# Kernel optimization log

Measured on AMD Instinct MI355X. Metric: run time of the kernel, lower is better.

Reference implementation:

```python
import jax, jax.numpy as jnp
import numpy as np
from math import factorial

DEGREES = 6
REP = 10
PROJ = 64
R = 0.8
B = DEGREES + 1          # bandwidth; spherical signal grid is (2B, 2B)
M = (DEGREES + 1) ** 2   # 49 spherical-harmonic coefficients

# ---------- Wigner small-d coefficient tables (numpy, per degree) ----------

def _wigner_terms(l):
    idx_mp, idx_m, coef, pc, ps = [], [], [], [], []
    for mp in range(-l, l + 1):
        for m in range(-l, l + 1):
            pref = np.sqrt(float(factorial(l + mp) * factorial(l - mp) * factorial(l + m) * factorial(l - m)))
            for k in range(max(0, m - mp), min(l + m, l - mp) + 1):
                c = ((-1.0) ** (mp - m + k)) * pref / (
                    factorial(l + m - k) * factorial(k) * factorial(l - mp - k) * factorial(mp - m + k))
                idx_mp.append(mp + l); idx_m.append(m + l); coef.append(c)
                pc.append(2 * l + m - mp - 2 * k); ps.append(mp - m + 2 * k)
    return (np.asarray(idx_mp), np.asarray(idx_m), np.asarray(coef, np.float32),
            np.asarray(pc, np.float32), np.asarray(ps, np.float32))

_TERMS = [_wigner_terms(l) for l in range(DEGREES + 1)]


def _wigner_d(l, beta):
    """Real Wigner small-d matrix d^l_{m',m}(beta): (n, 2l+1, 2l+1)."""
    imp, im, coef, pc, ps = _TERMS[l]
    c = jnp.cos(beta / 2)[:, None]
    s = jnp.sin(beta / 2)[:, None]
    t = coef[None] * (c ** pc[None]) * (s ** ps[None])   # (n, T)
    d = jnp.zeros((beta.shape[0], 2 * l + 1, 2 * l + 1), beta.dtype)
    return d.at[:, imp, im].add(t)


def rotate_spectrum(angles, spectrum):
    """Block-diagonal complex Wigner-D multiply.
    angles: (n,3) ZYZ Euler; spectrum: (M, rep, 2) -> (Sre, Sim) each (n, M, rep)."""
    alpha, beta, gamma = angles[:, 0], angles[:, 1], angles[:, 2]
    out_re, out_im = [], []
    for l in range(DEGREES + 1):
        d = _wigner_d(l, beta)                                    # (n, 2l+1, 2l+1)
        ms = jnp.arange(-l, l + 1, dtype=angles.dtype)
        ang = ms[None, :, None] * alpha[:, None, None] + ms[None, None, :] * gamma[:, None, None]
        Dre = d * jnp.cos(ang)
        Dim = -d * jnp.sin(ang)                                   # D = e^{-i m' a} d e^{-i m g}
        blk = spectrum[l * l:(l + 1) * (l + 1)]                   # (2l+1, rep, 2)
        Sre, Sim = blk[..., 0], blk[..., 1]
        out_re.append(jnp.einsum('nij,jr->nir', Dre, Sre) - jnp.einsum('nij,jr->nir', Dim, Sim))
        out_im.append(jnp.einsum('nij,jr->nir', Dre, Sim) + jnp.einsum('nij,jr->nir', Dim, Sre))
    return jnp.concatenate(out_re, 1), jnp.concatenate(out_im, 1)


# ---------- Spherical harmonic synthesis table (numpy constant) ----------

def _sph_harm_table():
    J = 2 * B
    betas = np.pi * (2 * np.arange(J) + 1) / (4 * B)
    alphas = 2 * np.pi * np.arange(J) / J
    x, sx = np.cos(betas), np.sin(betas)
    L = DEGREES
    P = np.zeros((L + 1, L + 1, J))   # associated Legendre P[l, m] (Condon-Shortley)
    P[0, 0] = 1.0
    for m in range(1, L + 1):
        P[m, m] = -(2 * m - 1) * sx * P[m - 1, m - 1]
    for m in range(L + 1):
        if m + 1 <= L:
            P[m + 1, m] = (2 * m + 1) * x * P[m, m]
        for l in range(m + 2, L + 1):
            P[l, m] = ((2 * l - 1) * x * P[l - 1, m] - (l + m - 1) * P[l - 2, m]) / (l - m)
    Yre = np.zeros((M, J, J)); Yim = np.zeros((M, J, J))
    for l in range(L + 1):
        for m in range(0, l + 1):
            N = np.sqrt((2 * l + 1) / (4 * np.pi) * factorial(l - m) / factorial(l + m))
            pr = N * P[l, m]
            yre = pr[:, None] * np.cos(m * alphas)[None, :]
            yim = pr[:, None] * np.sin(m * alphas)[None, :]
            Yre[l * l + l + m], Yim[l * l + l + m] = yre, yim
            if m > 0:
                sgn = (-1.0) ** m
                Yre[l * l + l - m], Yim[l * l + l - m] = sgn * yre, -sgn * yim
    return jnp.asarray(Yre, jnp.float32), jnp.asarray(Yim, jnp.float32)

_YRE, _YIM = _sph_harm_table()


def s2_ifft_real(Sre, Sim):
    """f(beta,alpha) = Re[sum_lm c_lm Y_lm]: (n, rep, 2B, 2B)."""
    return jnp.einsum('nmr,mjk->nrjk', Sre, _YRE) - jnp.einsum('nmr,mjk->nrjk', Sim, _YIM)


# ---------- Orthographic sampling grid (numpy constant) ----------

def _ortho_grid(h, w, r):
    ys, xs = np.meshgrid(np.linspace(-r, r, h), np.linspace(-r, r, w), indexing='ij')
    rho = np.sqrt(xs ** 2 + ys ** 2)
    theta = np.arcsin(np.clip(rho, 0.0, 1.0))     # colatitude of front hemisphere
    phi = np.arctan2(ys, xs)                      # longitude in [-pi, pi)
    gx = phi / np.pi                              # alpha axis  -> grid x
    gy = 2 * theta / np.pi - 1                    # beta axis   -> grid y
    return jnp.asarray(np.stack([gx, gy], -1), jnp.float32)

_GRID = _ortho_grid(PROJ, PROJ, R)


def grid_sample_bilinear(img, grid):
    """F.grid_sample(mode=bilinear, padding=zeros, align_corners=False).
    img: (n,C,H,W); grid: (Ho,Wo,2) shared across batch."""
    n, C, H, W = img.shape
    gx = (grid[..., 0] + 1) * W / 2 - 0.5
    gy = (grid[..., 1] + 1) * H / 2 - 0.5
    x0 = jnp.floor(gx); y0 = jnp.floor(gy)
    wx1 = gx - x0; wx0 = 1 - wx1
    wy1 = gy - y0; wy0 = 1 - wy1

    def gather(xi, yi, w):
        valid = (xi >= 0) & (xi < W) & (yi >= 0) & (yi < H)
        xc = jnp.clip(xi, 0, W - 1).astype(jnp.int32)
        yc = jnp.clip(yi, 0, H - 1).astype(jnp.int32)
        vals = img[:, :, yc, xc]                 # (n, C, Ho, Wo)
        return vals * (w * valid)[None, None]
    return (gather(x0, y0, wx0 * wy0) + gather(x0 + 1, y0, wx1 * wy0)
            + gather(x0, y0 + 1, wx0 * wy1) + gather(x0 + 1, y0 + 1, wx1 * wy1))


def deconv_apply(x, wt, bt):
    """ConvTranspose2d(REP,1,kernel=4,stride=2,padding=1); wt torch layout (Cin,Cout,4,4)."""
    k = jnp.transpose(wt[:, :, ::-1, ::-1], (1, 0, 2, 3))   # (Cout,Cin,kh,kw), flipped
    y = jax.lax.conv_general_dilated(x, k, window_strides=(1, 1),
                                     padding=((2, 2), (2, 2)), lhs_dilation=(2, 2),
                                     dimension_numbers=('NCHW', 'OIHW', 'NCHW'))
    return y + bt[None, :, None, None]


def setup_inputs() -> dict:
    key = jax.random.key(0)
    k1, k2, k3 = jax.random.split(key, 3)
    return {
        'angles': jax.random.uniform(k1, (2048, 3), dtype=jnp.float32),
        'spectrum': jax.random.normal(k2, (M, REP, 2), dtype=jnp.float32),
        'wt': jax.random.normal(k3, (REP, 1, 4, 4), dtype=jnp.float32) * 0.1,
        'bt': jnp.zeros((1,), jnp.float32),
    }


def reference(angles, spectrum, wt, bt):
    Sre, Sim = rotate_spectrum(angles, spectrum)        # (n, M, rep) complex parts
    signal = s2_ifft_real(Sre, Sim)                     # (n, rep, 14, 14)
    projection = grid_sample_bilinear(signal, _GRID)    # (n, rep, 64, 64)
    return deconv_apply(projection, wt, bt)             # (n, 1, 128, 128)
```

## Files before the change

kernel.cpp:

```cpp
#include <hip/hip_runtime.h>
#include <math.h>

#define DEG   6
#define MM    49
#define REPC  10
#define JD    14
#define JROWS 8
#define PROJD 64

#define PI_F 3.14159265358979323846f
#define PI_D 3.14159265358979323846

#define WS_GW    0
#define WS_GIDX  17688
#define WS_PT    22112
#define WS_CS    22504
#define WS_FLAG  22700
#define INIT_MAGIC 0x5F3A9C74u

__device__ __constant__ int DOFF[8] = {0,1,10,35,84,165,286,455};
__device__ __constant__ float FACTF[13] = {
    1.f,1.f,2.f,6.f,24.f,120.f,720.f,5040.f,40320.f,362880.f,
    3628800.f,39916800.f,479001600.f};
__device__ __constant__ double FACTD[13] = {
    1.,1.,2.,6.,24.,120.,720.,5040.,40320.,362880.,3628800.,39916800.,479001600.};

__device__ inline float ipowf(float b, int e) {
    float r = 1.f, p = b;
    while (e) { if (e & 1) r *= p; p *= p; e >>= 1; }
    return r;
}

__global__ void init_tables(float* __restrict__ ws) {
    if (*(const volatile unsigned int*)(ws + WS_FLAG) == INIT_MAGIC) return;
    const int tid = blockIdx.x * 256 + threadIdx.x;

    if (tid < 4422) {
        const int ty = tid / 66, tx = tid - ty * 66;
        const int iy = ty - 1, ix = tx - 1;
        float4 wv = make_float4(0.f, 0.f, 0.f, 0.f);
        unsigned int bidx = 0u;
        if ((unsigned)iy < 64u && (unsigned)ix < 64u) {
            float ys = -0.8f + 1.6f * (float)iy / 63.f;
            float xs = -0.8f + 1.6f * (float)ix / 63.f;
            float rho = sqrtf(xs * xs + ys * ys);
            float theta = asinf(fminf(rho, 1.0f));
            float phi = atan2f(ys, xs);
            float gxp = (phi / PI_F + 1.f) * 7.f - 0.5f;
            float gyp = (2.f * theta / PI_F) * 7.f - 0.5f;
            float x0f = floorf(gxp), y0f = floorf(gyp);
            int x0 = (int)x0f, y0 = (int)y0f;
            float fx = gxp - x0f, fy = gyp - y0f;
            float wx0 = 1.f - fx, wx1 = fx, wy0 = 1.f - fy, wy1 = fy;
            int xb = x0, yb = y0;
            if (x0 < 0)            { xb = 0; wx0 = wx1; wx1 = 0.f; }
            else if (x0 >= JD - 1) { wx1 = 0.f; }
            if (y0 < 0)            { yb = 0; wy0 = wy1; wy1 = 0.f; }
            wv = make_float4(wy0*wx0, wy0*wx1, wy1*wx0, wy1*wx1);
            bidx = (unsigned int)((xb * 8 + yb) * 17);
        }
        ((float4*)(ws + WS_GW))[tid] = wv;
        ((unsigned int*)(ws + WS_GIDX))[tid] = bidx;
    }

    const int t2 = tid - 4422;
    if (t2 >= 0 && t2 < JROWS) {
        const int j = t2;
        double bj = PI_D * (2.0 * j + 1.0) / 28.0;
        double x = cos(bj), sx = sin(bj);
        double P[7][7];
        P[0][0] = 1.0;
        for (int m = 1; m <= 6; ++m) P[m][m] = -(2.0*m - 1.0) * sx * P[m-1][m-1];
        for (int m = 0; m <= 6; ++m) {
            if (m + 1 <= 6) P[m+1][m] = (2.0*m + 1.0) * x * P[m][m];
            for (int l = m + 2; l <= 6; ++l)
                P[l][m] = ((2.0*l - 1.0)*x*P[l-1][m] - (double)(l+m-1)*P[l-2][m])
                          / (double)(l - m);
        }
        for (int l = 0; l <= 6; ++l)
            for (int m = 0; m <= 6; ++m) {
                float v = 0.f;
                if (m <= l) {
                    double N = sqrt((2.0*l + 1.0)/(4.0*PI_D) * FACTD[l-m]/FACTD[l+m]);
                    v = (float)(N * P[l][m]);
                }
                ws[WS_PT + j*49 + l*7 + m] = v;
            }
    } else if (t2 >= JROWS && t2 < JROWS + JD) {
        const int k = t2 - JROWS;
        for (int mu = 0; mu <= 6; ++mu) {
            double ang = 2.0 * PI_D * (double)k * (double)mu / 14.0;
            ws[WS_CS + (k*7 + mu)*2 + 0] = (float)cos(ang);
            ws[WS_CS + (k*7 + mu)*2 + 1] = (float)sin(ang);
        }
    }
}

__device__ __forceinline__ float tap4(const float* __restrict__ T, int b, int c,
                                      float4 w) {
    int a = b + c;
    return fmaf(w.x, T[a],
           fmaf(w.y, T[a + 136],
           fmaf(w.z, T[a + 17],
                w.w * T[a + 153])));
}

__global__ __launch_bounds__(256, 8) void fused_decode(
    const float* __restrict__ angles,
    const float* __restrict__ spectrum,
    const float* __restrict__ wt,
    const float* __restrict__ bt,
    float* __restrict__ out,
    const float* __restrict__ ws) {
    const int n = blockIdx.x;
    const int tid = threadIdx.x;

    __shared__ __align__(16) float2 Ss[490];
    __shared__ __align__(16) float  T16p[2040];
    __shared__ __align__(16) float  bufU[1772];

    float*  sigL  = bufU;
    float*  dmatL = bufU + 1120;
    float2* CsL   = (float2*)(bufU + 1576);
    float*  specL = T16p;
    float2* ABL   = (float2*)T16p;
    float*  wLcS  = (float*)Ss;

    const float alpha = angles[n*3 + 0];
    const float beta  = angles[n*3 + 1];
    const float gamma = angles[n*3 + 2];

    if (tid < 245) ((float4*)specL)[tid] = ((const float4*)spectrum)[tid];
    if (tid < 49)  ((float4*)CsL)[tid]   = ((const float4*)(ws + WS_CS))[tid];

    {
        float cb = cosf(beta * 0.5f), sb = sinf(beta * 0.5f);
        float ratio = (sb * sb) / (cb * cb);
        for (int idx = tid; idx < 455; idx += 256) {
            int l = 0;
            while (idx >= DOFF[l+1]) ++l;
            int tl = 2*l + 1;
            int loc = idx - DOFF[l];
            int mp = loc / tl - l;
            int m  = loc % tl - l;
            float pref = sqrtf(FACTF[l+mp]*FACTF[l-mp]*FACTF[l+m]*FACTF[l-m]);
            int k0 = max(0, m - mp), k1 = min(l + m, l - mp);
            float p = ipowf(cb, 2*l + m - mp - 2*k0) * ipowf(sb, mp - m + 2*k0);
            float dsum = 0.f;
            for (int k = k0; k <= k1; ++k) {
                float c = pref / (FACTF[l+m-k]*FACTF[k]*FACTF[l-mp-k]*FACTF[mp-m+k]);
                if ((mp - m + k) & 1) c = -c;
                dsum += c * p;
                p *= ratio;
            }
            dmatL[idx] = dsum;
        }
    }
    __syncthreads();

    {
        float cg, sg; sincosf(gamma, &sg, &cg);
        for (int idx = tid; idx < 490; idx += 256) {
            int lm = idx / 10, r = idx - lm*10;
            int l = 0; { while ((l+1)*(l+1) <= lm) ++l; }
            int mp = lm - l*l - l;
            int tl = 2*l + 1;
            const float* drow = dmatL + DOFF[l] + (mp + l)*tl;
            float ca, sa; sincosf((float)mp*alpha - (float)l*gamma, &sa, &ca);
            float sre = 0.f, sim = 0.f;
            const float* sp = specL + (l*l)*20 + r*2;
            for (int mi = 0; mi < tl; ++mi) {
                float d = drow[mi];
                float Dre = d * ca, Dim = -d * sa;
                float vr = sp[mi*20], vi = sp[mi*20 + 1];
                sre += Dre*vr - Dim*vi;
                sim += Dre*vi + Dim*vr;
                float ca2 = ca*cg - sa*sg;
                float sa2 = sa*cg + ca*sg;
                ca = ca2; sa = sa2;
            }
            Ss[lm*10 + r] = make_float2(sre, sim);
        }
    }
    __syncthreads();

    for (int idx = tid; idx < 560; idx += 256) {
        int r = idx % 10;
        int jm = idx / 10;
        int j = jm / 7, mu = jm - j*7;
        float sgn = (mu & 1) ? -1.f : 1.f;
        const float* pt = ws + WS_PT + j*49 + mu;
        float A = 0.f, B = 0.f;
        #pragma unroll
        for (int l = 0; l <= 6; ++l) {
            float P = pt[l*7];
            int base = l*l + l;
            int im = base - mu; im = im < 0 ? 0 : im;
            float2 spv = Ss[(base + mu)*10 + r];
            float2 snv = Ss[im*10 + r];
            A += P * (spv.x + sgn*snv.x);
            B += P * (sgn*snv.y - spv.y);
        }
        float sc = (mu == 0) ? 0.5f : 1.f;
        ABL[idx] = make_float2(A*sc, B*sc);
    }
    __syncthreads();

    if (tid < 40) ((float4*)wLcS)[tid] = ((const float4*)wt)[tid];
    for (int idx = tid; idx < 1120; idx += 256) {
        int k = idx % 14;
        int t = idx / 14;
        int j = t & 7, r = t >> 3;
        const float2* ab = ABL + j*70 + r;
        const float2* cs = CsL + k*7;
        float acc = 0.f;
        #pragma unroll
        for (int mu = 0; mu <= 6; ++mu) {
            float2 a = ab[mu*10];
            float2 c = cs[mu];
            acc += a.x*c.x + a.y*c.y;
        }
        sigL[idx] = acc;
    }
    __syncthreads();

    for (int idx = tid; idx < 1920; idx += 256) {
        int c = idx & 15, p = idx >> 4;
        int j = p / 15, k = p - j*15;
        float acc = 0.f;
        if (k < 14) {
            const float* sl = sigL + j*14 + k;
            const float* wc = wLcS + c;
            #pragma unroll
            for (int r = 0; r < REPC; ++r)
                acc += wc[r*16] * sl[r*112];
        }
        T16p[(k*8 + j)*17 + c] = acc;
    }
    __syncthreads();

    const float btv = bt[0];
    const int wv   = tid >> 6;
    const int lane = tid & 63;
    const int pxp  = wv & 1;
    const int qy0  = wv >> 1;
    const int qx   = 2*lane + pxp;
    const int ixh  = lane + pxp;
    const int kxh  = 1 - pxp;
    const int kyh  = 1 - qy0;
    const int iyh0 = qy0;
    const int cN0 = kyh*4 + kxh, cN1 = cN0 + 2;
    const int cO0 = cN0 + 8,     cO1 = cN0 + 10;

    const unsigned int* gI = (const unsigned int*)(ws + WS_GIDX);
    const float4* gWt = (const float4*)(ws + WS_GW);

    int ridx = iyh0 * 66 + (ixh + 1);
    float4 wA0 = gWt[ridx];   unsigned int bA0 = gI[ridx];
    float4 wB0 = gWt[ridx-1]; unsigned int bB0 = gI[ridx-1];
    ridx += 66;
    float4 wA1 = gWt[ridx];   unsigned int bA1 = gI[ridx];
    float4 wB1 = gWt[ridx-1]; unsigned int bB1 = gI[ridx-1];
    ridx += 66;
    float4 wA2 = gWt[ridx];   unsigned int bA2 = gI[ridx];
    float4 wB2 = gWt[ridx-1]; unsigned int bB2 = gI[ridx-1];

    float* op = out + (size_t)n * 16384 + qy0 * 128 + qx;

    for (int t = 0; t < 63; t += 3) {
        {
            float o = btv + tap4(T16p, bA1, cN0, wA1) + tap4(T16p, bB1, cN1, wB1)
                          + tap4(T16p, bA0, cO0, wA0) + tap4(T16p, bB0, cO1, wB0);
            __builtin_nontemporal_store(o, op); op += 256;
            ridx += 66;
            wA0 = gWt[ridx]; bA0 = gI[ridx]; wB0 = gWt[ridx-1]; bB0 = gI[ridx-1];
        }
        {
            float o = btv + tap4(T16p, bA2, cN0, wA2) + tap4(T16p, bB2, cN1, wB2)
                          + tap4(T16p, bA1, cO0, wA1) + tap4(T16p, bB1, cO1, wB1);
            __builtin_nontemporal_store(o, op); op += 256;
            ridx += 66;
            wA1 = gWt[ridx]; bA1 = gI[ridx]; wB1 = gWt[ridx-1]; bB1 = gI[ridx-1];
        }
        {
            float o = btv + tap4(T16p, bA0, cN0, wA0) + tap4(T16p, bB0, cN1, wB0)
                          + tap4(T16p, bA2, cO0, wA2) + tap4(T16p, bB2, cO1, wB2);
            __builtin_nontemporal_store(o, op); op += 256;
            ridx += 66;
            wA2 = gWt[ridx]; bA2 = gI[ridx]; wB2 = gWt[ridx-1]; bB2 = gI[ridx-1];
        }
    }
    {
        float o = btv + tap4(T16p, bA1, cN0, wA1) + tap4(T16p, bB1, cN1, wB1)
                      + tap4(T16p, bA0, cO0, wA0) + tap4(T16p, bB0, cO1, wB0);
        __builtin_nontemporal_store(o, op);
    }

    if (n == 0 && tid == 0)
        *((volatile unsigned int*)(ws + WS_FLAG)) = INIT_MAGIC;
}

extern "C" void kernel_launch(void* const* d_in, const int* in_sizes, int n_in,
                              void* d_out, int out_size, void* d_ws, size_t ws_size,
                              hipStream_t stream) {
    const float* angles   = nullptr;
    const float* spectrum = nullptr;
    const float* wt       = nullptr;
    const float* bt       = nullptr;
    int n = 2048;
    for (int i = 0; i < n_in; ++i) {
        int sz = in_sizes[i];
        if (sz == 980)      spectrum = (const float*)d_in[i];
        else if (sz == 160) wt = (const float*)d_in[i];
        else if (sz == 1)   bt = (const float*)d_in[i];
        else { angles = (const float*)d_in[i]; n = sz / 3; }
    }
    float* out = (float*)d_out;
    float* ws  = (float*)d_ws;
    (void)ws_size;

    init_tables<<<18, 256, 0, stream>>>(ws);
    fused_decode<<<n, 256, 0, stream>>>(angles, spectrum, wt, bt, out, ws);
}
```

Measured before the change: 225.1 us.

## Restructure deconv output so each lane computes an even/odd pixel pair

Each lane now produces two horizontally adjacent output pixels, written as one 8-byte nontemporal store. The four waves split the output rows by vertical parity and by upper/lower half, instead of by horizontal parity. Three adjacent cell records per row are reused across both pixels, and tap offsets become compile-time template constants. This is meant to cut global loads of the grid tables, store instruction count and address arithmetic per output, at the cost of more registers held per lane.

```diff
diff --git a/kernel.cpp b/kernel.cpp
--- a/kernel.cpp
+++ b/kernel.cpp
@@ -10,6 +10,8 @@
 
 #define PI_F 3.14159265358979323846f
 #define PI_D 3.14159265358979323846
+
+typedef float f32x2 __attribute__((ext_vector_type(2)));
 
 #define WS_GW    0
 #define WS_GIDX  17688
@@ -96,13 +98,68 @@
     }
 }
 
-__device__ __forceinline__ float tap4(const float* __restrict__ T, int b, int c,
-                                      float4 w) {
-    int a = b + c;
-    return fmaf(w.x, T[a],
-           fmaf(w.y, T[a + 136],
-           fmaf(w.z, T[a + 17],
-                w.w * T[a + 153])));
+struct CellRec { float4 w; unsigned int b; };
+__device__ __forceinline__ CellRec ldrec(const float4* __restrict__ gWt,
+                                         const unsigned int* __restrict__ gI,
+                                         int idx) {
+    CellRec r; r.w = gWt[idx]; r.b = gI[idx]; return r;
+}
+
+template<int C>
+__device__ __forceinline__ float tap4c(const float* __restrict__ T,
+                                       unsigned int b, float4 w) {
+    return fmaf(w.x, T[b + C],
+           fmaf(w.y, T[b + C + 136],
+           fmaf(w.z, T[b + C + 17],
+                w.w * T[b + C + 153])));
+}
+
+template<int KYH>
+__device__ __forceinline__ void backhalf(
+    const float* __restrict__ T16p, const float4* __restrict__ gWt,
+    const unsigned int* __restrict__ gI, f32x2* __restrict__ op,
+    int rbase, float btv) {
+    constexpr int CE0 = KYH*4 + 1, CE1 = CE0 + 2, CE2 = CE0 + 8, CE3 = CE0 + 10;
+    constexpr int CO0 = KYH*4,     CO1 = CO0 + 2, CO2 = CO0 + 8, CO3 = CO0 + 10;
+
+    CellRec a0 = ldrec(gWt, gI, rbase), a1 = ldrec(gWt, gI, rbase + 1),
+            a2 = ldrec(gWt, gI, rbase + 2);
+    int rn = rbase + 66;
+    CellRec b0 = ldrec(gWt, gI, rn), b1 = ldrec(gWt, gI, rn + 1),
+            b2 = ldrec(gWt, gI, rn + 2);
+
+    for (int i = 0; i < 16; ++i) {
+        {
+            float oe = btv + tap4c<CE0>(T16p, b1.b, b1.w)
+                           + tap4c<CE1>(T16p, b0.b, b0.w)
+                           + tap4c<CE2>(T16p, a1.b, a1.w)
+                           + tap4c<CE3>(T16p, a0.b, a0.w);
+            float oo = btv + tap4c<CO0>(T16p, b2.b, b2.w)
+                           + tap4c<CO1>(T16p, b1.b, b1.w)
+                           + tap4c<CO2>(T16p, a2.b, a2.w)
+                           + tap4c<CO3>(T16p, a1.b, a1.w);
+            f32x2 o2; o2.x = oe; o2.y = oo;
+            __builtin_nontemporal_store(o2, op); op += 128;
+        }
+        rn += 66;
+        a0 = ldrec(gWt, gI, rn); a1 = ldrec(gWt, gI, rn + 1);
+        a2 = ldrec(gWt, gI, rn + 2);
+        {
+            float oe = btv + tap4c<CE0>(T16p, a1.b, a1.w)
+                           + tap4c<CE1>(T16p, a0.b, a0.w)
+                           + tap4c<CE2>(T16p, b1.b, b1.w)
+                           + tap4c<CE3>(T16p, b0.b, b0.w);
+            float oo = btv + tap4c<CO0>(T16p, a2.b, a2.w)
+                           + tap4c<CO1>(T16p, a1.b, a1.w)
+                           + tap4c<CO2>(T16p, b2.b, b2.w)
+                           + tap4c<CO3>(T16p, b1.b, b1.w);
+            f32x2 o2; o2.x = oe; o2.y = oo;
+            __builtin_nontemporal_store(o2, op); op += 128;
+        }
+        rn += 66;
+        b0 = ldrec(gWt, gI, rn); b1 = ldrec(gWt, gI, rn + 1);
+        b2 = ldrec(gWt, gI, rn + 2);
+    }
 }
 
 __global__ __launch_bounds__(256, 8) void fused_decode(
@@ -242,59 +299,17 @@
     const float btv = bt[0];
     const int wv   = tid >> 6;
     const int lane = tid & 63;
-    const int pxp  = wv & 1;
     const int qy0  = wv >> 1;
-    const int qx   = 2*lane + pxp;
-    const int ixh  = lane + pxp;
-    const int kxh  = 1 - pxp;
-    const int kyh  = 1 - qy0;
-    const int iyh0 = qy0;
-    const int cN0 = kyh*4 + kxh, cN1 = cN0 + 2;
-    const int cO0 = cN0 + 8,     cO1 = cN0 + 10;
+    const int half = wv & 1;
+    const int t0   = half * 32;
+    const int rbase = (t0 + qy0) * 66 + lane;
 
     const unsigned int* gI = (const unsigned int*)(ws + WS_GIDX);
     const float4* gWt = (const float4*)(ws + WS_GW);
-
-    int ridx = iyh0 * 66 + (ixh + 1);
-    float4 wA0 = gWt[ridx];   unsigned int bA0 = gI[ridx];
-    float4 wB0 = gWt[ridx-1]; unsigned int bB0 = gI[ridx-1];
-    ridx += 66;
-    float4 wA1 = gWt[ridx];   unsigned int bA1 = gI[ridx];
-    float4 wB1 = gWt[ridx-1]; unsigned int bB1 = gI[ridx-1];
-    ridx += 66;
-    float4 wA2 = gWt[ridx];   unsigned int bA2 = gI[ridx];
-    float4 wB2 = gWt[ridx-1]; unsigned int bB2 = gI[ridx-1];
-
-    float* op = out + (size_t)n * 16384 + qy0 * 128 + qx;
-
-    for (int t = 0; t < 63; t += 3) {
-        {
-            float o = btv + tap4(T16p, bA1, cN0, wA1) + tap4(T16p, bB1, cN1, wB1)
-                          + tap4(T16p, bA0, cO0, wA0) + tap4(T16p, bB0, cO1, wB0);
-            __builtin_nontemporal_store(o, op); op += 256;
-            ridx += 66;
-            wA0 = gWt[ridx]; bA0 = gI[ridx]; wB0 = gWt[ridx-1]; bB0 = gI[ridx-1];
-        }
-        {
-            float o = btv + tap4(T16p, bA2, cN0, wA2) + tap4(T16p, bB2, cN1, wB2)
-                          + tap4(T16p, bA1, cO0, wA1) + tap4(T16p, bB1, cO1, wB1);
-            __builtin_nontemporal_store(o, op); op += 256;
-            ridx += 66;
-            wA1 = gWt[ridx]; bA1 = gI[ridx]; wB1 = gWt[ridx-1]; bB1 = gI[ridx-1];
-        }
-        {
-            float o = btv + tap4(T16p, bA0, cN0, wA0) + tap4(T16p, bB0, cN1, wB0)
-                          + tap4(T16p, bA2, cO0, wA2) + tap4(T16p, bB2, cO1, wB2);
-            __builtin_nontemporal_store(o, op); op += 256;
-            ridx += 66;
-            wA2 = gWt[ridx]; bA2 = gI[ridx]; wB2 = gWt[ridx-1]; bB2 = gI[ridx-1];
-        }
-    }
-    {
-        float o = btv + tap4(T16p, bA1, cN0, wA1) + tap4(T16p, bB1, cN1, wB1)
-                      + tap4(T16p, bA0, cO0, wA0) + tap4(T16p, bB0, cO1, wB0);
-        __builtin_nontemporal_store(o, op);
-    }
+    f32x2* op = (f32x2*)out + (size_t)n * 8192 + (size_t)(qy0 + 2*t0) * 64 + lane;
+
+    if (qy0 == 0) backhalf<1>(T16p, gWt, gI, op, rbase, btv);
+    else          backhalf<0>(T16p, gWt, gI, op, rbase, btv);
 
     if (n == 0 && tid == 0)
         *((volatile unsigned int*)(ws + WS_FLAG)) = INIT_MAGIC;
```

New measurement: 196.0 us. -13.0%, faster.
